# Kernel optimization log

Hardware: AMD Instinct MI355X
Metric: run time of the kernel (lower is better)

The kernel has to match this reference:

```python
import jax, jax.numpy as jnp
import numpy as np

B, T = 256, 512
D_L, D_T, D_W, D_S = 64, 32, 32, 32
XPRIME, HIDDEN = 256, 512


def setup_inputs() -> dict:
    key = jax.random.key(0)
    ks = jax.random.split(key, 11)
    s = 0.05
    return {
        "x_l_seq": jax.random.normal(ks[0], (B, T, D_L), jnp.float32),
        "x_t_seq": jax.random.normal(ks[1], (B, T, D_T), jnp.float32),
        "x_w_seq": jax.random.normal(ks[2], (B, T, D_W), jnp.float32),
        "x_s_seq": jax.random.normal(ks[3], (B, T, D_S), jnp.float32),
        "W_ih": jax.random.normal(ks[4], (3 * HIDDEN, XPRIME), jnp.float32) * s,
        "W_hh": jax.random.normal(ks[5], (3 * HIDDEN, HIDDEN), jnp.float32) * s,
        "b_ih": jax.random.normal(ks[6], (3 * HIDDEN,), jnp.float32) * s,
        "b_hh": jax.random.normal(ks[7], (3 * HIDDEN,), jnp.float32) * s,
        "Wt_h": jax.random.normal(ks[8], (XPRIME, HIDDEN), jnp.float32) * s,
        "Wt_x": jax.random.normal(ks[9], (XPRIME, D_L + D_T + D_W + D_S), jnp.float32) * s,
        "bt": jax.random.normal(ks[10], (XPRIME,), jnp.float32) * s,
    }


def reference(x_l_seq, x_t_seq, x_w_seq, x_s_seq, W_ih, W_hh, b_ih, b_hh, Wt_h, Wt_x, bt):
    # concat the four feature streams once: [B, T, D_tot]
    x_cat = jnp.concatenate([x_l_seq, x_t_seq, x_w_seq, x_s_seq], axis=-1)
    H = W_hh.shape[1]
    Bb = x_cat.shape[0]

    def step(h, x_t):  # h: [B,H], x_t: [B,D_tot]
        # transform_block: per-step meta transform fused with recurrence
        x_prime = jnp.tanh(h @ Wt_h.T + x_t @ Wt_x.T + bt)  # [B, XPRIME]
        # torch nn.GRU cell (gate order r, z, n)
        gx = x_prime @ W_ih.T + b_ih  # [B, 3H]
        gh = h @ W_hh.T + b_hh        # [B, 3H]
        xr, xz, xn = gx[:, :H], gx[:, H:2 * H], gx[:, 2 * H:]
        hr, hz, hn = gh[:, :H], gh[:, H:2 * H], gh[:, 2 * H:]
        r = jax.nn.sigmoid(xr + hr)
        z = jax.nn.sigmoid(xz + hz)
        n = jnp.tanh(xn + r * hn)
        h_new = (1.0 - z) * n + z * h
        return h_new, None

    h0 = jnp.zeros((Bb, H), x_cat.dtype)
    hT, _ = jax.lax.scan(step, h0, jnp.swapaxes(x_cat, 0, 1))  # scan over T
    return hT[None, :, :]  # [num_layers=1, B, H]
```

## Files before the change

### kernel.cpp

```cpp
#include <hip/hip_runtime.h>
#include <math.h>

typedef __attribute__((ext_vector_type(8))) short short8;
typedef __attribute__((ext_vector_type(4))) float floatx4;
typedef __attribute__((ext_vector_type(4))) unsigned uintx4;

#define NB 256
#define NH 512
#define NXP 256
#define NT 512
#define GHP 100

#define MFMA __builtin_amdgcn_mfma_f32_16x16x32_bf16

__device__ __forceinline__ unsigned short f2bf(float f) {
    union { float f; unsigned u; } x; x.f = f;
    unsigned r = x.u + 0x7FFFu + ((x.u >> 16) & 1u);
    return (unsigned short)(r >> 16);
}
__device__ __forceinline__ float sigmoidf_(float x) { return 1.0f / (1.0f + __expf(-x)); }

__device__ __forceinline__ short8 cvt8(float4 u, float4 v) {
    short8 r;
    r[0] = (short)f2bf(u.x); r[1] = (short)f2bf(u.y);
    r[2] = (short)f2bf(u.z); r[3] = (short)f2bf(u.w);
    r[4] = (short)f2bf(v.x); r[5] = (short)f2bf(v.y);
    r[6] = (short)f2bf(v.z); r[7] = (short)f2bf(v.w);
    return r;
}

__device__ __forceinline__ void ldg4_c(const void* p0, const void* p1,
                                       const void* p2, const void* p3,
                                       uintx4& r0, uintx4& r1, uintx4& r2, uintx4& r3) {
    asm volatile(
        "global_load_dwordx4 %0, %4, off sc0 sc1\n\t"
        "global_load_dwordx4 %1, %5, off sc0 sc1\n\t"
        "global_load_dwordx4 %2, %6, off sc0 sc1\n\t"
        "global_load_dwordx4 %3, %7, off sc0 sc1\n\t"
        "s_waitcnt vmcnt(0)"
        : "=&v"(r0), "=&v"(r1), "=&v"(r2), "=&v"(r3)
        : "v"(p0), "v"(p1), "v"(p2), "v"(p3) : "memory");
}
__device__ __forceinline__ void ldg2_c(const void* p0, const void* p1,
                                       uintx4& r0, uintx4& r1) {
    asm volatile(
        "global_load_dwordx4 %0, %2, off sc0 sc1\n\t"
        "global_load_dwordx4 %1, %3, off sc0 sc1\n\t"
        "s_waitcnt vmcnt(0)"
        : "=&v"(r0), "=&v"(r1) : "v"(p0), "v"(p1) : "memory");
}
__device__ __forceinline__ void st16_c(void* p, unsigned v) {
    asm volatile("global_store_short %0, %1, off sc0 sc1" :: "v"(p), "v"(v) : "memory");
}
__device__ __forceinline__ void st32_c(void* p, unsigned v) {
    asm volatile("global_store_dword %0, %1, off sc0 sc1" :: "v"(p), "v"(v) : "memory");
}
__device__ __forceinline__ void vm_drain() {
    asm volatile("s_waitcnt vmcnt(0)" ::: "memory");
}

__device__ __forceinline__ void flag_set(int* f, int v) {
    __hip_atomic_store(f, v, __ATOMIC_RELAXED, __HIP_MEMORY_SCOPE_AGENT);
}
__device__ __forceinline__ void poll16(const int* f, int target, int lane) {
    const int* fp = f + (lane & 15) * 16;
    for (;;) {
        int v = __hip_atomic_load(fp, __ATOMIC_RELAXED, __HIP_MEMORY_SCOPE_AGENT);
        if (__ballot(v < target) == 0ull) break;
        __builtin_amdgcn_s_sleep(1);
    }
}

__global__ void k_cvt(const float* __restrict__ src, unsigned short* __restrict__ dst, int n) {
    int i = blockIdx.x * blockDim.x + threadIdx.x;
    int stride = gridDim.x * blockDim.x;
    for (; i < n; i += stride) dst[i] = f2bf(src[i]);
}

struct KParams {
    const float *xl, *xt, *xw, *xs;
    const float *bih, *bhh, *bt;
    const unsigned short *Wihb, *Whhb, *Wthb, *Wtxb;
    unsigned short *hb0, *hb1, *xpb;
    float *out;
    int *flags;
};

__global__ __launch_bounds__(256, 1)
void k_persist(KParams P)
{
    const int tid   = threadIdx.x;
    const int w     = tid >> 6;
    const int lane  = tid & 63;
    const int lr    = lane & 15;
    const int lkrow = lane >> 4;
    const int lk    = lkrow * 8;
    const int bid   = blockIdx.x;
    const int grp   = bid >> 4;
    const int jc    = bid & 15;
    const int m0    = grp * 16;
    const int j0    = jc * 32;
    const int n0    = jc * 16;

    int* gfl = P.flags + grp * 512;
    int* hfl = gfl;
    int* xfl = gfl + 256;

    __shared__ unsigned short sh_h[16 * 512];
    __shared__ unsigned short sh_xp[16 * 256];
    __shared__ float sh_gh[16 * GHP];
    __shared__ float sh_gx[2][16 * GHP];
    __shared__ float sh_hf[16 * 32];
    __shared__ float sh_b[6][32];
    __shared__ float sh_bt[16];

    if (tid < 32) {
        sh_b[0][tid] = P.bih[j0 + tid];
        sh_b[1][tid] = P.bih[512 + j0 + tid];
        sh_b[2][tid] = P.bih[1024 + j0 + tid];
        sh_b[3][tid] = P.bhh[j0 + tid];
        sh_b[4][tid] = P.bhh[512 + j0 + tid];
        sh_b[5][tid] = P.bhh[1024 + j0 + tid];
    }
    if (tid < 16) sh_bt[tid] = P.bt[n0 + tid];
    sh_hf[tid] = 0.f; sh_hf[tid + 256] = 0.f;

    short8 bWih[3][4];
    short8 bWhh[2][16];
    #pragma unroll
    for (int i = 0; i < 3; ++i) {
        const int u = w * 3 + i, tile = u >> 1, kh = u & 1;
        const int g = tile >> 1, sub = tile & 1;
        const unsigned short* bp =
            P.Wihb + (size_t)(g * 512 + j0 + sub * 16 + lr) * NXP + kh * 128 + lk;
        #pragma unroll
        for (int kb = 0; kb < 4; ++kb) bWih[i][kb] = *(const short8*)(bp + kb * 32);
    }
    if (w < 3) {
        #pragma unroll
        for (int sub = 0; sub < 2; ++sub) {
            const unsigned short* bp =
                P.Whhb + (size_t)(w * 512 + j0 + sub * 16 + lr) * NH + lk;
            #pragma unroll
            for (int kb = 0; kb < 16; ++kb) bWhh[sub][kb] = *(const short8*)(bp + kb * 32);
        }
    } else {
        const unsigned short* bp = P.Wthb + (size_t)(n0 + lr) * NH + lk;
        #pragma unroll
        for (int kb = 0; kb < 16; ++kb) bWhh[0][kb] = *(const short8*)(bp + kb * 32);
        const unsigned short* bx = P.Wtxb + (size_t)(n0 + lr) * 160 + lk;
        #pragma unroll
        for (int c = 0; c < 5; ++c) bWhh[1][c] = *(const short8*)(bx + c * 32);
    }
    __syncthreads();

    for (int t = 0; t < NT; ++t) {
        const unsigned short* hsrc = (t & 1) ? P.hb1 : P.hb0;
        unsigned short*       hdst = (t & 1) ? P.hb0 : P.hb1;

        float4 xq[5][2];
        if (w == 3) {
            const size_t r = (size_t)(m0 + lr);
            #pragma unroll
            for (int c = 0; c < 5; ++c) {
                const float* pa = (c < 2) ? P.xl + (r * NT + t) * 64 + c * 32 + lk
                                : (c == 2)? P.xt + (r * NT + t) * 32 + lk
                                : (c == 3)? P.xw + (r * NT + t) * 32 + lk
                                          : P.xs + (r * NT + t) * 32 + lk;
                xq[c][0] = *(const float4*)pa;
                xq[c][1] = *(const float4*)(pa + 4);
            }
        }

        poll16(hfl, t, lane);
        {
            const int row = tid >> 4, c = (tid & 15) * 32;
            const unsigned short* gp = hsrc + (size_t)(m0 + row) * NH + c;
            uintx4 r0, r1, r2, r3;
            ldg4_c(gp, gp + 8, gp + 16, gp + 24, r0, r1, r2, r3);
            const int sw = (row & 7) * 8;
            *(uintx4*)&sh_h[row * 512 + ((c +  0) ^ sw)] = r0;
            *(uintx4*)&sh_h[row * 512 + ((c +  8) ^ sw)] = r1;
            *(uintx4*)&sh_h[row * 512 + ((c + 16) ^ sw)] = r2;
            *(uintx4*)&sh_h[row * 512 + ((c + 24) ^ sw)] = r3;
        }
        __syncthreads();

        if (w < 3) {
            floatx4 a0 = (floatx4){0.f,0.f,0.f,0.f};
            floatx4 a1 = (floatx4){0.f,0.f,0.f,0.f};
            const int sw = (lr & 7) * 8;
            #pragma unroll
            for (int kb = 0; kb < 16; ++kb) {
                short8 a = *(const short8*)&sh_h[lr * 512 + ((kb * 32 + lk) ^ sw)];
                a0 = MFMA(a, bWhh[0][kb], a0, 0, 0, 0);
                a1 = MFMA(a, bWhh[1][kb], a1, 0, 0, 0);
            }
            #pragma unroll
            for (int rg = 0; rg < 4; ++rg) {
                const int row = lkrow * 4 + rg;
                sh_gh[row * GHP + w * 32 + lr]      = a0[rg];
                sh_gh[row * GHP + w * 32 + 16 + lr] = a1[rg];
            }
        } else {
            floatx4 acc = (floatx4){0.f,0.f,0.f,0.f};
            const int sw = (lr & 7) * 8;
            #pragma unroll
            for (int kb = 0; kb < 16; ++kb) {
                short8 a = *(const short8*)&sh_h[lr * 512 + ((kb * 32 + lk) ^ sw)];
                acc = MFMA(a, bWhh[0][kb], acc, 0, 0, 0);
            }
            #pragma unroll
            for (int c = 0; c < 5; ++c) {
                short8 a = cvt8(xq[c][0], xq[c][1]);
                acc = MFMA(a, bWhh[1][c], acc, 0, 0, 0);
            }
            #pragma unroll
            for (int rg = 0; rg < 4; ++rg) {
                const int row = lkrow * 4 + rg;
                unsigned short v = f2bf(tanhf(acc[rg] + sh_bt[lr]));
                st16_c(P.xpb + (size_t)(m0 + row) * NXP + n0 + lr, (unsigned)v);
            }
            vm_drain();
            if (lane == 0) flag_set(xfl + jc * 16, t + 1);
        }

        poll16(xfl, t + 1, lane);
        {
            const int row = tid >> 4, c = (tid & 15) * 16;
            const unsigned short* gp = P.xpb + (size_t)(m0 + row) * NXP + c;
            uintx4 r0, r1;
            ldg2_c(gp, gp + 8, r0, r1);
            const int sw = (row & 7) * 8;
            *(uintx4*)&sh_xp[row * 256 + ((c + 0) ^ sw)] = r0;
            *(uintx4*)&sh_xp[row * 256 + ((c + 8) ^ sw)] = r1;
        }
        __syncthreads();

        #pragma unroll
        for (int i = 0; i < 3; ++i) {
            const int u = w * 3 + i, tile = u >> 1, kh = u & 1;
            const int g = tile >> 1, sub = tile & 1;
            floatx4 acc = (floatx4){0.f,0.f,0.f,0.f};
            const int sw = (lr & 7) * 8;
            #pragma unroll
            for (int kb = 0; kb < 4; ++kb) {
                short8 a = *(const short8*)&sh_xp[lr * 256 + ((kh * 128 + kb * 32 + lk) ^ sw)];
                acc = MFMA(a, bWih[i][kb], acc, 0, 0, 0);
            }
            #pragma unroll
            for (int rg = 0; rg < 4; ++rg) {
                const int row = lkrow * 4 + rg;
                sh_gx[kh][row * GHP + g * 32 + sub * 16 + lr] = acc[rg];
            }
        }
        __syncthreads();

        {
            const int row = tid >> 4, jj = (tid & 15) * 2;
            float hn[2];
            #pragma unroll
            for (int jo = 0; jo < 2; ++jo) {
                const int j = jj + jo;
                float gxr = sh_gx[0][row * GHP + j]      + sh_gx[1][row * GHP + j];
                float gxz = sh_gx[0][row * GHP + 32 + j] + sh_gx[1][row * GHP + 32 + j];
                float gxn = sh_gx[0][row * GHP + 64 + j] + sh_gx[1][row * GHP + 64 + j];
                float ghr = sh_gh[row * GHP + j];
                float ghz = sh_gh[row * GHP + 32 + j];
                float ghn = sh_gh[row * GHP + 64 + j];
                float rg_ = sigmoidf_(gxr + ghr + sh_b[0][j] + sh_b[3][j]);
                float zg  = sigmoidf_(gxz + ghz + sh_b[1][j] + sh_b[4][j]);
                float ng  = tanhf(gxn + sh_b[2][j] + rg_ * (ghn + sh_b[5][j]));
                float hold = sh_hf[row * 32 + j];
                hn[jo] = (1.f - zg) * ng + zg * hold;
                sh_hf[row * 32 + j] = hn[jo];
            }
            unsigned d = (unsigned)f2bf(hn[0]) | ((unsigned)f2bf(hn[1]) << 16);
            st32_c(hdst + (size_t)(m0 + row) * NH + j0 + jj, d);
            if (t == NT - 1) {
                float2 o; o.x = hn[0]; o.y = hn[1];
                *(float2*)&P.out[(size_t)(m0 + row) * NH + j0 + jj] = o;
            }
            vm_drain();
        }
        __syncthreads();
        if (tid == 0) flag_set(hfl + jc * 16, t + 1);
    }
}

extern "C" void kernel_launch(void* const* d_in, const int* in_sizes, int n_in,
                              void* d_out, int out_size, void* d_ws, size_t ws_size,
                              hipStream_t stream)
{
    (void)in_sizes; (void)n_in; (void)out_size;
    const float* xl  = (const float*)d_in[0];
    const float* xt_ = (const float*)d_in[1];
    const float* xw  = (const float*)d_in[2];
    const float* xs  = (const float*)d_in[3];
    const float* Wih = (const float*)d_in[4];
    const float* Whh = (const float*)d_in[5];
    const float* bih = (const float*)d_in[6];
    const float* bhh = (const float*)d_in[7];
    const float* Wth = (const float*)d_in[8];
    const float* Wtx = (const float*)d_in[9];
    const float* bt  = (const float*)d_in[10];

    char* p = (char*)d_ws;
    int* flags = (int*)p;                       p += 32768;
    unsigned short* hb0 = (unsigned short*)p;   p += (size_t)NB * NH * 2;
    unsigned short* hb1 = (unsigned short*)p;   p += (size_t)NB * NH * 2;
    unsigned short* xpb = (unsigned short*)p;   p += (size_t)NB * NXP * 2;
    unsigned short* Wihb = (unsigned short*)p;  p += (size_t)1536 * 256 * 2;
    unsigned short* Whhb = (unsigned short*)p;  p += (size_t)1536 * 512 * 2;
    unsigned short* Wthb = (unsigned short*)p;  p += (size_t)256 * 512 * 2;
    unsigned short* Wtxb = (unsigned short*)p;  p += (size_t)256 * 160 * 2;
    if ((size_t)(p - (char*)d_ws) > ws_size) return;

    k_cvt<<<256, 256, 0, stream>>>(Wih, Wihb, 1536 * 256);
    k_cvt<<<256, 256, 0, stream>>>(Whh, Whhb, 1536 * 512);
    k_cvt<<<64, 256, 0, stream>>>(Wth, Wthb, 256 * 512);
    k_cvt<<<32, 256, 0, stream>>>(Wtx, Wtxb, 256 * 160);
    hipMemsetAsync(flags, 0, 32768, stream);
    hipMemsetAsync(hb0, 0, (size_t)NB * NH * 2, stream);

    KParams P;
    P.xl = xl; P.xt = xt_; P.xw = xw; P.xs = xs;
    P.bih = bih; P.bhh = bhh; P.bt = bt;
    P.Wihb = Wihb; P.Whhb = Whhb; P.Wthb = Wthb; P.Wtxb = Wtxb;
    P.hb0 = hb0; P.hb1 = hb1; P.xpb = xpb;
    P.out = (float*)d_out; P.flags = flags;

    void* args[] = { &P };
    if (hipLaunchCooperativeKernel((const void*)k_persist, dim3(256), dim3(256),
                                   args, 0, stream) != hipSuccess) {
        k_persist<<<256, 256, 0, stream>>>(P);
    }
}
```

Measured before the change: 3.244 ms.

## Use 128 blocks of 512 threads, each covering 64 hidden columns

Halves the grid to 128 persistent blocks with 8 waves each, so every block handles 64 hidden columns and 32 x-prime columns instead of 32 and 16. Flag polling now runs in a single wave followed by a block barrier, and each wave publishes its own h flag instead of one flag per block after a final barrier. The goal is fewer cross-block dependencies and flags per step, with each block sharing the staged h rows over more work. The cost is half as many CUs in use, more register pressure at launch_bounds(512,2), and extra __syncthreads per step.

```diff
diff --git a/kernel.cpp b/kernel.cpp
--- a/kernel.cpp
+++ b/kernel.cpp
@@ -9,7 +9,7 @@
 #define NH 512
 #define NXP 256
 #define NT 512
-#define GHP 100
+#define GH2 200
 
 #define MFMA __builtin_amdgcn_mfma_f32_16x16x32_bf16
 
@@ -29,18 +29,6 @@
     return r;
 }
 
-__device__ __forceinline__ void ldg4_c(const void* p0, const void* p1,
-                                       const void* p2, const void* p3,
-                                       uintx4& r0, uintx4& r1, uintx4& r2, uintx4& r3) {
-    asm volatile(
-        "global_load_dwordx4 %0, %4, off sc0 sc1\n\t"
-        "global_load_dwordx4 %1, %5, off sc0 sc1\n\t"
-        "global_load_dwordx4 %2, %6, off sc0 sc1\n\t"
-        "global_load_dwordx4 %3, %7, off sc0 sc1\n\t"
-        "s_waitcnt vmcnt(0)"
-        : "=&v"(r0), "=&v"(r1), "=&v"(r2), "=&v"(r3)
-        : "v"(p0), "v"(p1), "v"(p2), "v"(p3) : "memory");
-}
 __device__ __forceinline__ void ldg2_c(const void* p0, const void* p1,
                                        uintx4& r0, uintx4& r1) {
     asm volatile(
@@ -49,6 +37,12 @@
         "s_waitcnt vmcnt(0)"
         : "=&v"(r0), "=&v"(r1) : "v"(p0), "v"(p1) : "memory");
 }
+__device__ __forceinline__ void ldg1_c(const void* p0, uintx4& r0) {
+    asm volatile(
+        "global_load_dwordx4 %0, %1, off sc0 sc1\n\t"
+        "s_waitcnt vmcnt(0)"
+        : "=&v"(r0) : "v"(p0) : "memory");
+}
 __device__ __forceinline__ void st16_c(void* p, unsigned v) {
     asm volatile("global_store_short %0, %1, off sc0 sc1" :: "v"(p), "v"(v) : "memory");
 }
@@ -61,6 +55,14 @@
 
 __device__ __forceinline__ void flag_set(int* f, int v) {
     __hip_atomic_store(f, v, __ATOMIC_RELAXED, __HIP_MEMORY_SCOPE_AGENT);
+}
+__device__ __forceinline__ void poll64(const int* f, int target, int lane) {
+    const int* fp = f + lane * 16;
+    for (;;) {
+        int v = __hip_atomic_load(fp, __ATOMIC_RELAXED, __HIP_MEMORY_SCOPE_AGENT);
+        if (__ballot(v < target) == 0ull) break;
+        __builtin_amdgcn_s_sleep(1);
+    }
 }
 __device__ __forceinline__ void poll16(const int* f, int target, int lane) {
     const int* fp = f + (lane & 15) * 16;
@@ -86,7 +88,7 @@
     int *flags;
 };
 
-__global__ __launch_bounds__(256, 1)
+__global__ __launch_bounds__(512, 2)
 void k_persist(KParams P)
 {
     const int tid   = threadIdx.x;
@@ -96,25 +98,25 @@
     const int lkrow = lane >> 4;
     const int lk    = lkrow * 8;
     const int bid   = blockIdx.x;
-    const int grp   = bid >> 4;
-    const int jc    = bid & 15;
+    const int grp   = bid >> 3;
+    const int jc    = bid & 7;
     const int m0    = grp * 16;
-    const int j0    = jc * 32;
-    const int n0    = jc * 16;
-
-    int* gfl = P.flags + grp * 512;
+    const int j0    = jc * 64;
+    const int n0    = jc * 32;
+
+    int* gfl = P.flags + grp * 2048;
     int* hfl = gfl;
-    int* xfl = gfl + 256;
+    int* xfl = gfl + 1024;
 
     __shared__ unsigned short sh_h[16 * 512];
     __shared__ unsigned short sh_xp[16 * 256];
-    __shared__ float sh_gh[16 * GHP];
-    __shared__ float sh_gx[2][16 * GHP];
-    __shared__ float sh_hf[16 * 32];
-    __shared__ float sh_b[6][32];
-    __shared__ float sh_bt[16];
-
-    if (tid < 32) {
+    __shared__ float sh_gh[16 * GH2];
+    __shared__ float sh_gx[2][16 * GH2];
+    __shared__ float sh_hf[16 * 64];
+    __shared__ float sh_b[6][64];
+    __shared__ float sh_bt[32];
+
+    if (tid < 64) {
         sh_b[0][tid] = P.bih[j0 + tid];
         sh_b[1][tid] = P.bih[512 + j0 + tid];
         sh_b[2][tid] = P.bih[1024 + j0 + tid];
@@ -122,35 +124,37 @@
         sh_b[4][tid] = P.bhh[512 + j0 + tid];
         sh_b[5][tid] = P.bhh[1024 + j0 + tid];
     }
-    if (tid < 16) sh_bt[tid] = P.bt[n0 + tid];
-    sh_hf[tid] = 0.f; sh_hf[tid + 256] = 0.f;
+    if (tid < 32) sh_bt[tid] = P.bt[n0 + tid];
+    sh_hf[tid] = 0.f; sh_hf[tid + 512] = 0.f;
 
     short8 bWih[3][4];
-    short8 bWhh[2][16];
+    short8 bW[2][16];
     #pragma unroll
     for (int i = 0; i < 3; ++i) {
         const int u = w * 3 + i, tile = u >> 1, kh = u & 1;
-        const int g = tile >> 1, sub = tile & 1;
+        const int g = tile >> 2, sub = tile & 3;
         const unsigned short* bp =
             P.Wihb + (size_t)(g * 512 + j0 + sub * 16 + lr) * NXP + kh * 128 + lk;
         #pragma unroll
         for (int kb = 0; kb < 4; ++kb) bWih[i][kb] = *(const short8*)(bp + kb * 32);
     }
-    if (w < 3) {
+    if (w < 6) {
+        const int g = w >> 1, cp = w & 1;
         #pragma unroll
         for (int sub = 0; sub < 2; ++sub) {
             const unsigned short* bp =
-                P.Whhb + (size_t)(w * 512 + j0 + sub * 16 + lr) * NH + lk;
-            #pragma unroll
-            for (int kb = 0; kb < 16; ++kb) bWhh[sub][kb] = *(const short8*)(bp + kb * 32);
+                P.Whhb + (size_t)(g * 512 + j0 + cp * 32 + sub * 16 + lr) * NH + lk;
+            #pragma unroll
+            for (int kb = 0; kb < 16; ++kb) bW[sub][kb] = *(const short8*)(bp + kb * 32);
         }
     } else {
-        const unsigned short* bp = P.Wthb + (size_t)(n0 + lr) * NH + lk;
-        #pragma unroll
-        for (int kb = 0; kb < 16; ++kb) bWhh[0][kb] = *(const short8*)(bp + kb * 32);
-        const unsigned short* bx = P.Wtxb + (size_t)(n0 + lr) * 160 + lk;
-        #pragma unroll
-        for (int c = 0; c < 5; ++c) bWhh[1][c] = *(const short8*)(bx + c * 32);
+        const int n = n0 + (w - 6) * 16;
+        const unsigned short* bp = P.Wthb + (size_t)(n + lr) * NH + lk;
+        #pragma unroll
+        for (int kb = 0; kb < 16; ++kb) bW[0][kb] = *(const short8*)(bp + kb * 32);
+        const unsigned short* bx = P.Wtxb + (size_t)(n + lr) * 160 + lk;
+        #pragma unroll
+        for (int c = 0; c < 5; ++c) bW[1][c] = *(const short8*)(bx + c * 32);
     }
     __syncthreads();
 
@@ -159,7 +163,7 @@
         unsigned short*       hdst = (t & 1) ? P.hb0 : P.hb1;
 
         float4 xq[5][2];
-        if (w == 3) {
+        if (w >= 6) {
             const size_t r = (size_t)(m0 + lr);
             #pragma unroll
             for (int c = 0; c < 5; ++c) {
@@ -172,35 +176,35 @@
             }
         }
 
-        poll16(hfl, t, lane);
+        if (w == 0) poll64(hfl, t, lane);
+        __syncthreads();
         {
-            const int row = tid >> 4, c = (tid & 15) * 32;
+            const int row = tid >> 5, c = (tid & 31) * 16;
             const unsigned short* gp = hsrc + (size_t)(m0 + row) * NH + c;
-            uintx4 r0, r1, r2, r3;
-            ldg4_c(gp, gp + 8, gp + 16, gp + 24, r0, r1, r2, r3);
+            uintx4 r0, r1;
+            ldg2_c(gp, gp + 8, r0, r1);
             const int sw = (row & 7) * 8;
-            *(uintx4*)&sh_h[row * 512 + ((c +  0) ^ sw)] = r0;
-            *(uintx4*)&sh_h[row * 512 + ((c +  8) ^ sw)] = r1;
-            *(uintx4*)&sh_h[row * 512 + ((c + 16) ^ sw)] = r2;
-            *(uintx4*)&sh_h[row * 512 + ((c + 24) ^ sw)] = r3;
-        }
-        __syncthreads();
-
-        if (w < 3) {
+            *(uintx4*)&sh_h[row * 512 + ((c + 0) ^ sw)] = r0;
+            *(uintx4*)&sh_h[row * 512 + ((c + 8) ^ sw)] = r1;
+        }
+        __syncthreads();
+
+        if (w < 6) {
+            const int g = w >> 1, cp = w & 1;
             floatx4 a0 = (floatx4){0.f,0.f,0.f,0.f};
             floatx4 a1 = (floatx4){0.f,0.f,0.f,0.f};
             const int sw = (lr & 7) * 8;
             #pragma unroll
             for (int kb = 0; kb < 16; ++kb) {
                 short8 a = *(const short8*)&sh_h[lr * 512 + ((kb * 32 + lk) ^ sw)];
-                a0 = MFMA(a, bWhh[0][kb], a0, 0, 0, 0);
-                a1 = MFMA(a, bWhh[1][kb], a1, 0, 0, 0);
+                a0 = MFMA(a, bW[0][kb], a0, 0, 0, 0);
+                a1 = MFMA(a, bW[1][kb], a1, 0, 0, 0);
             }
             #pragma unroll
             for (int rg = 0; rg < 4; ++rg) {
                 const int row = lkrow * 4 + rg;
-                sh_gh[row * GHP + w * 32 + lr]      = a0[rg];
-                sh_gh[row * GHP + w * 32 + 16 + lr] = a1[rg];
+                sh_gh[row * GH2 + g * 64 + cp * 32 + lr]      = a0[rg];
+                sh_gh[row * GH2 + g * 64 + cp * 32 + 16 + lr] = a1[rg];
             }
         } else {
             floatx4 acc = (floatx4){0.f,0.f,0.f,0.f};
@@ -208,39 +212,40 @@
             #pragma unroll
             for (int kb = 0; kb < 16; ++kb) {
                 short8 a = *(const short8*)&sh_h[lr * 512 + ((kb * 32 + lk) ^ sw)];
-                acc = MFMA(a, bWhh[0][kb], acc, 0, 0, 0);
+                acc = MFMA(a, bW[0][kb], acc, 0, 0, 0);
             }
             #pragma unroll
             for (int c = 0; c < 5; ++c) {
                 short8 a = cvt8(xq[c][0], xq[c][1]);
-                acc = MFMA(a, bWhh[1][c], acc, 0, 0, 0);
-            }
+                acc = MFMA(a, bW[1][c], acc, 0, 0, 0);
+            }
+            const int xcol = n0 + (w - 6) * 16 + lr;
             #pragma unroll
             for (int rg = 0; rg < 4; ++rg) {
                 const int row = lkrow * 4 + rg;
-                unsigned short v = f2bf(tanhf(acc[rg] + sh_bt[lr]));
-                st16_c(P.xpb + (size_t)(m0 + row) * NXP + n0 + lr, (unsigned)v);
+                unsigned short v = f2bf(tanhf(acc[rg] + sh_bt[(w - 6) * 16 + lr]));
+                st16_c(P.xpb + (size_t)(m0 + row) * NXP + xcol, (unsigned)v);
             }
             vm_drain();
-            if (lane == 0) flag_set(xfl + jc * 16, t + 1);
-        }
-
-        poll16(xfl, t + 1, lane);
+            if (lane == 0) flag_set(xfl + (jc * 2 + (w - 6)) * 16, t + 1);
+        }
+
+        if (w == 0) poll16(xfl, t + 1, lane);
+        __syncthreads();
         {
-            const int row = tid >> 4, c = (tid & 15) * 16;
+            const int row = tid >> 5, c = (tid & 31) * 8;
             const unsigned short* gp = P.xpb + (size_t)(m0 + row) * NXP + c;
-            uintx4 r0, r1;
-            ldg2_c(gp, gp + 8, r0, r1);
+            uintx4 r0;
+            ldg1_c(gp, r0);
             const int sw = (row & 7) * 8;
-            *(uintx4*)&sh_xp[row * 256 + ((c + 0) ^ sw)] = r0;
-            *(uintx4*)&sh_xp[row * 256 + ((c + 8) ^ sw)] = r1;
+            *(uintx4*)&sh_xp[row * 256 + (c ^ sw)] = r0;
         }
         __syncthreads();
 
         #pragma unroll
         for (int i = 0; i < 3; ++i) {
             const int u = w * 3 + i, tile = u >> 1, kh = u & 1;
-            const int g = tile >> 1, sub = tile & 1;
+            const int g = tile >> 2, sub = tile & 3;
             floatx4 acc = (floatx4){0.f,0.f,0.f,0.f};
             const int sw = (lr & 7) * 8;
             #pragma unroll
@@ -251,40 +256,39 @@
             #pragma unroll
             for (int rg = 0; rg < 4; ++rg) {
                 const int row = lkrow * 4 + rg;
-                sh_gx[kh][row * GHP + g * 32 + sub * 16 + lr] = acc[rg];
+                sh_gx[kh][row * GH2 + g * 64 + sub * 16 + lr] = acc[rg];
             }
         }
         __syncthreads();
 
         {
-            const int row = tid >> 4, jj = (tid & 15) * 2;
+            const int row = tid >> 5, jl = (tid & 31) * 2;
             float hn[2];
             #pragma unroll
             for (int jo = 0; jo < 2; ++jo) {
-                const int j = jj + jo;
-                float gxr = sh_gx[0][row * GHP + j]      + sh_gx[1][row * GHP + j];
-                float gxz = sh_gx[0][row * GHP + 32 + j] + sh_gx[1][row * GHP + 32 + j];
-                float gxn = sh_gx[0][row * GHP + 64 + j] + sh_gx[1][row * GHP + 64 + j];
-                float ghr = sh_gh[row * GHP + j];
-                float ghz = sh_gh[row * GHP + 32 + j];
-                float ghn = sh_gh[row * GHP + 64 + j];
+                const int j = jl + jo;
+                float gxr = sh_gx[0][row * GH2 + j]       + sh_gx[1][row * GH2 + j];
+                float gxz = sh_gx[0][row * GH2 + 64 + j]  + sh_gx[1][row * GH2 + 64 + j];
+                float gxn = sh_gx[0][row * GH2 + 128 + j] + sh_gx[1][row * GH2 + 128 + j];
+                float ghr = sh_gh[row * GH2 + j];
+                float ghz = sh_gh[row * GH2 + 64 + j];
+                float ghn = sh_gh[row * GH2 + 128 + j];
                 float rg_ = sigmoidf_(gxr + ghr + sh_b[0][j] + sh_b[3][j]);
                 float zg  = sigmoidf_(gxz + ghz + sh_b[1][j] + sh_b[4][j]);
                 float ng  = tanhf(gxn + sh_b[2][j] + rg_ * (ghn + sh_b[5][j]));
-                float hold = sh_hf[row * 32 + j];
+                float hold = sh_hf[row * 64 + j];
                 hn[jo] = (1.f - zg) * ng + zg * hold;
-                sh_hf[row * 32 + j] = hn[jo];
+                sh_hf[row * 64 + j] = hn[jo];
             }
             unsigned d = (unsigned)f2bf(hn[0]) | ((unsigned)f2bf(hn[1]) << 16);
-            st32_c(hdst + (size_t)(m0 + row) * NH + j0 + jj, d);
+            st32_c(hdst + (size_t)(m0 + row) * NH + j0 + jl, d);
             if (t == NT - 1) {
                 float2 o; o.x = hn[0]; o.y = hn[1];
-                *(float2*)&P.out[(size_t)(m0 + row) * NH + j0 + jj] = o;
+                *(float2*)&P.out[(size_t)(m0 + row) * NH + j0 + jl] = o;
             }
             vm_drain();
-        }
-        __syncthreads();
-        if (tid == 0) flag_set(hfl + jc * 16, t + 1);
+            if (lane == 0) flag_set(hfl + (jc * 8 + w) * 16, t + 1);
+        }
     }
 }
 
@@ -306,7 +310,7 @@
     const float* bt  = (const float*)d_in[10];
 
     char* p = (char*)d_ws;
-    int* flags = (int*)p;                       p += 32768;
+    int* flags = (int*)p;                       p += 16 * 2048 * 4;
     unsigned short* hb0 = (unsigned short*)p;   p += (size_t)NB * NH * 2;
     unsigned short* hb1 = (unsigned short*)p;   p += (size_t)NB * NH * 2;
     unsigned short* xpb = (unsigned short*)p;   p += (size_t)NB * NXP * 2;
@@ -320,7 +324,7 @@
     k_cvt<<<256, 256, 0, stream>>>(Whh, Whhb, 1536 * 512);
     k_cvt<<<64, 256, 0, stream>>>(Wth, Wthb, 256 * 512);
     k_cvt<<<32, 256, 0, stream>>>(Wtx, Wtxb, 256 * 160);
-    hipMemsetAsync(flags, 0, 32768, stream);
+    hipMemsetAsync(flags, 0, 16 * 2048 * 4, stream);
     hipMemsetAsync(hb0, 0, (size_t)NB * NH * 2, stream);
 
     KParams P;
@@ -331,8 +335,8 @@
     P.out = (float*)d_out; P.flags = flags;
 
     void* args[] = { &P };
-    if (hipLaunchCooperativeKernel((const void*)k_persist, dim3(256), dim3(256),
+    if (hipLaunchCooperativeKernel((const void*)k_persist, dim3(128), dim3(512),
                                    args, 0, stream) != hipSuccess) {
-        k_persist<<<256, 256, 0, stream>>>(P);
-    }
-}
+        k_persist<<<128, 512, 0, stream>>>(P);
+    }
+}
```

After: 3.794 ms. 17.0% more time.

## Replace flag-based inter-block sync with tag-embedded data polling

Applied to the files above, without the earlier changes.

Removes the separate flag arrays and the store-drain-flag handshake between blocks. Each bf16 value of h and x_prime is now stored in a 32-bit word whose upper 16 bits carry the step tag, and consumers poll the data itself until every word carries the expected tag, then repack to bf16 in shared memory. This cuts a round trip (drain, flag write, flag poll, then data load) from the critical path of every step, and also drops the trailing __syncthreads. In exchange it doubles the size of the exchanged buffers and adds repeated polling loads. Correctness rests on the tag staying unique across the double buffer; the 16-bit tag only ever reaches 512, so that holds here.

```diff
diff --git a/kernel.cpp b/kernel.cpp
--- a/kernel.cpp
+++ b/kernel.cpp
@@ -29,46 +29,15 @@
     return r;
 }
 
-__device__ __forceinline__ void ldg4_c(const void* p0, const void* p1,
-                                       const void* p2, const void* p3,
-                                       uintx4& r0, uintx4& r1, uintx4& r2, uintx4& r3) {
-    asm volatile(
-        "global_load_dwordx4 %0, %4, off sc0 sc1\n\t"
-        "global_load_dwordx4 %1, %5, off sc0 sc1\n\t"
-        "global_load_dwordx4 %2, %6, off sc0 sc1\n\t"
-        "global_load_dwordx4 %3, %7, off sc0 sc1\n\t"
-        "s_waitcnt vmcnt(0)"
-        : "=&v"(r0), "=&v"(r1), "=&v"(r2), "=&v"(r3)
-        : "v"(p0), "v"(p1), "v"(p2), "v"(p3) : "memory");
-}
-__device__ __forceinline__ void ldg2_c(const void* p0, const void* p1,
-                                       uintx4& r0, uintx4& r1) {
-    asm volatile(
-        "global_load_dwordx4 %0, %2, off sc0 sc1\n\t"
-        "global_load_dwordx4 %1, %3, off sc0 sc1\n\t"
-        "s_waitcnt vmcnt(0)"
-        : "=&v"(r0), "=&v"(r1) : "v"(p0), "v"(p1) : "memory");
-}
-__device__ __forceinline__ void st16_c(void* p, unsigned v) {
-    asm volatile("global_store_short %0, %1, off sc0 sc1" :: "v"(p), "v"(v) : "memory");
+__device__ __forceinline__ void ldg4_nw(const void* p, uintx4& r) {
+    asm volatile("global_load_dwordx4 %0, %1, off sc0 sc1"
+                 : "=&v"(r) : "v"(p) : "memory");
 }
 __device__ __forceinline__ void st32_c(void* p, unsigned v) {
     asm volatile("global_store_dword %0, %1, off sc0 sc1" :: "v"(p), "v"(v) : "memory");
 }
 __device__ __forceinline__ void vm_drain() {
     asm volatile("s_waitcnt vmcnt(0)" ::: "memory");
-}
-
-__device__ __forceinline__ void flag_set(int* f, int v) {
-    __hip_atomic_store(f, v, __ATOMIC_RELAXED, __HIP_MEMORY_SCOPE_AGENT);
-}
-__device__ __forceinline__ void poll16(const int* f, int target, int lane) {
-    const int* fp = f + (lane & 15) * 16;
-    for (;;) {
-        int v = __hip_atomic_load(fp, __ATOMIC_RELAXED, __HIP_MEMORY_SCOPE_AGENT);
-        if (__ballot(v < target) == 0ull) break;
-        __builtin_amdgcn_s_sleep(1);
-    }
 }
 
 __global__ void k_cvt(const float* __restrict__ src, unsigned short* __restrict__ dst, int n) {
@@ -81,9 +50,8 @@
     const float *xl, *xt, *xw, *xs;
     const float *bih, *bhh, *bt;
     const unsigned short *Wihb, *Whhb, *Wthb, *Wtxb;
-    unsigned short *hb0, *hb1, *xpb;
+    unsigned *hT0, *hT1, *xT;
     float *out;
-    int *flags;
 };
 
 __global__ __launch_bounds__(256, 1)
@@ -102,10 +70,6 @@
     const int j0    = jc * 32;
     const int n0    = jc * 16;
 
-    int* gfl = P.flags + grp * 512;
-    int* hfl = gfl;
-    int* xfl = gfl + 256;
-
     __shared__ unsigned short sh_h[16 * 512];
     __shared__ unsigned short sh_xp[16 * 256];
     __shared__ float sh_gh[16 * GHP];
@@ -155,8 +119,8 @@
     __syncthreads();
 
     for (int t = 0; t < NT; ++t) {
-        const unsigned short* hsrc = (t & 1) ? P.hb1 : P.hb0;
-        unsigned short*       hdst = (t & 1) ? P.hb0 : P.hb1;
+        const unsigned* hTs = (t & 1) ? P.hT1 : P.hT0;
+        unsigned*       hTd = (t & 1) ? P.hT0 : P.hT1;
 
         float4 xq[5][2];
         if (w == 3) {
@@ -172,17 +136,38 @@
             }
         }
 
-        poll16(hfl, t, lane);
         {
             const int row = tid >> 4, c = (tid & 15) * 32;
-            const unsigned short* gp = hsrc + (size_t)(m0 + row) * NH + c;
-            uintx4 r0, r1, r2, r3;
-            ldg4_c(gp, gp + 8, gp + 16, gp + 24, r0, r1, r2, r3);
+            const unsigned* bp = hTs + (size_t)(m0 + row) * NH + c;
+            uintx4 B[8];
+            unsigned pend = 0xFFu;
+            const unsigned tg = (unsigned)t;
+            for (;;) {
+                #pragma unroll
+                for (int b = 0; b < 8; ++b)
+                    if (pend & (1u << b)) ldg4_nw(bp + b * 4, B[b]);
+                vm_drain();
+                __builtin_amdgcn_sched_barrier(0);
+                #pragma unroll
+                for (int b = 0; b < 8; ++b)
+                    if (pend & (1u << b)) {
+                        if ((B[b][0] >> 16) == tg && (B[b][1] >> 16) == tg &&
+                            (B[b][2] >> 16) == tg && (B[b][3] >> 16) == tg)
+                            pend &= ~(1u << b);
+                    }
+                if (__ballot(pend != 0u) == 0ull) break;
+                __builtin_amdgcn_s_sleep(1);
+            }
             const int sw = (row & 7) * 8;
-            *(uintx4*)&sh_h[row * 512 + ((c +  0) ^ sw)] = r0;
-            *(uintx4*)&sh_h[row * 512 + ((c +  8) ^ sw)] = r1;
-            *(uintx4*)&sh_h[row * 512 + ((c + 16) ^ sw)] = r2;
-            *(uintx4*)&sh_h[row * 512 + ((c + 24) ^ sw)] = r3;
+            #pragma unroll
+            for (int q = 0; q < 4; ++q) {
+                uintx4 pk;
+                pk[0] = (B[2*q][0]   & 0xffffu) | (B[2*q][1]   << 16);
+                pk[1] = (B[2*q][2]   & 0xffffu) | (B[2*q][3]   << 16);
+                pk[2] = (B[2*q+1][0] & 0xffffu) | (B[2*q+1][1] << 16);
+                pk[3] = (B[2*q+1][2] & 0xffffu) | (B[2*q+1][3] << 16);
+                *(uintx4*)&sh_h[row * 512 + ((c + 8 * q) ^ sw)] = pk;
+            }
         }
         __syncthreads();
 
@@ -215,25 +200,47 @@
                 short8 a = cvt8(xq[c][0], xq[c][1]);
                 acc = MFMA(a, bWhh[1][c], acc, 0, 0, 0);
             }
+            const unsigned xtag = ((unsigned)(t + 1)) << 16;
             #pragma unroll
             for (int rg = 0; rg < 4; ++rg) {
                 const int row = lkrow * 4 + rg;
                 unsigned short v = f2bf(tanhf(acc[rg] + sh_bt[lr]));
-                st16_c(P.xpb + (size_t)(m0 + row) * NXP + n0 + lr, (unsigned)v);
-            }
-            vm_drain();
-            if (lane == 0) flag_set(xfl + jc * 16, t + 1);
-        }
-
-        poll16(xfl, t + 1, lane);
+                st32_c(P.xT + (size_t)(m0 + row) * NXP + n0 + lr, xtag | (unsigned)v);
+            }
+        }
+
         {
             const int row = tid >> 4, c = (tid & 15) * 16;
-            const unsigned short* gp = P.xpb + (size_t)(m0 + row) * NXP + c;
-            uintx4 r0, r1;
-            ldg2_c(gp, gp + 8, r0, r1);
+            const unsigned* bp = P.xT + (size_t)(m0 + row) * NXP + c;
+            uintx4 B[4];
+            unsigned pend = 0xFu;
+            const unsigned tg = (unsigned)(t + 1);
+            for (;;) {
+                #pragma unroll
+                for (int b = 0; b < 4; ++b)
+                    if (pend & (1u << b)) ldg4_nw(bp + b * 4, B[b]);
+                vm_drain();
+                __builtin_amdgcn_sched_barrier(0);
+                #pragma unroll
+                for (int b = 0; b < 4; ++b)
+                    if (pend & (1u << b)) {
+                        if ((B[b][0] >> 16) == tg && (B[b][1] >> 16) == tg &&
+                            (B[b][2] >> 16) == tg && (B[b][3] >> 16) == tg)
+                            pend &= ~(1u << b);
+                    }
+                if (__ballot(pend != 0u) == 0ull) break;
+                __builtin_amdgcn_s_sleep(1);
+            }
             const int sw = (row & 7) * 8;
-            *(uintx4*)&sh_xp[row * 256 + ((c + 0) ^ sw)] = r0;
-            *(uintx4*)&sh_xp[row * 256 + ((c + 8) ^ sw)] = r1;
+            #pragma unroll
+            for (int q = 0; q < 2; ++q) {
+                uintx4 pk;
+                pk[0] = (B[2*q][0]   & 0xffffu) | (B[2*q][1]   << 16);
+                pk[1] = (B[2*q][2]   & 0xffffu) | (B[2*q][3]   << 16);
+                pk[2] = (B[2*q+1][0] & 0xffffu) | (B[2*q+1][1] << 16);
+                pk[3] = (B[2*q+1][2] & 0xffffu) | (B[2*q+1][3] << 16);
+                *(uintx4*)&sh_xp[row * 256 + ((c + 8 * q) ^ sw)] = pk;
+            }
         }
         __syncthreads();
 
@@ -275,16 +282,15 @@
                 hn[jo] = (1.f - zg) * ng + zg * hold;
                 sh_hf[row * 32 + j] = hn[jo];
             }
-            unsigned d = (unsigned)f2bf(hn[0]) | ((unsigned)f2bf(hn[1]) << 16);
-            st32_c(hdst + (size_t)(m0 + row) * NH + j0 + jj, d);
+            const unsigned htag = ((unsigned)(t + 1)) << 16;
+            unsigned* hp = hTd + (size_t)(m0 + row) * NH + j0 + jj;
+            st32_c(hp,     htag | (unsigned)f2bf(hn[0]));
+            st32_c(hp + 1, htag | (unsigned)f2bf(hn[1]));
             if (t == NT - 1) {
                 float2 o; o.x = hn[0]; o.y = hn[1];
                 *(float2*)&P.out[(size_t)(m0 + row) * NH + j0 + jj] = o;
             }
-            vm_drain();
-        }
-        __syncthreads();
-        if (tid == 0) flag_set(hfl + jc * 16, t + 1);
+        }
     }
 }
 
@@ -306,10 +312,9 @@
     const float* bt  = (const float*)d_in[10];
 
     char* p = (char*)d_ws;
-    int* flags = (int*)p;                       p += 32768;
-    unsigned short* hb0 = (unsigned short*)p;   p += (size_t)NB * NH * 2;
-    unsigned short* hb1 = (unsigned short*)p;   p += (size_t)NB * NH * 2;
-    unsigned short* xpb = (unsigned short*)p;   p += (size_t)NB * NXP * 2;
+    unsigned* hT0 = (unsigned*)p;               p += (size_t)NB * NH * 4;
+    unsigned* hT1 = (unsigned*)p;               p += (size_t)NB * NH * 4;
+    unsigned* xT  = (unsigned*)p;               p += (size_t)NB * NXP * 4;
     unsigned short* Wihb = (unsigned short*)p;  p += (size_t)1536 * 256 * 2;
     unsigned short* Whhb = (unsigned short*)p;  p += (size_t)1536 * 512 * 2;
     unsigned short* Wthb = (unsigned short*)p;  p += (size_t)256 * 512 * 2;
@@ -320,15 +325,16 @@
     k_cvt<<<256, 256, 0, stream>>>(Whh, Whhb, 1536 * 512);
     k_cvt<<<64, 256, 0, stream>>>(Wth, Wthb, 256 * 512);
     k_cvt<<<32, 256, 0, stream>>>(Wtx, Wtxb, 256 * 160);
-    hipMemsetAsync(flags, 0, 32768, stream);
-    hipMemsetAsync(hb0, 0, (size_t)NB * NH * 2, stream);
+    hipMemsetAsync(hT0, 0, (size_t)NB * NH * 4, stream);
+    hipMemsetAsync(hT1, 0, (size_t)NB * NH * 4, stream);
+    hipMemsetAsync(xT,  0, (size_t)NB * NXP * 4, stream);
 
     KParams P;
     P.xl = xl; P.xt = xt_; P.xw = xw; P.xs = xs;
     P.bih = bih; P.bhh = bhh; P.bt = bt;
     P.Wihb = Wihb; P.Whhb = Whhb; P.Wthb = Wthb; P.Wtxb = Wtxb;
-    P.hb0 = hb0; P.hb1 = hb1; P.xpb = xpb;
-    P.out = (float*)d_out; P.flags = flags;
+    P.hT0 = hT0; P.hT1 = hT1; P.xT = xT;
+    P.out = (float*)d_out;
 
     void* args[] = { &P };
     if (hipLaunchCooperativeKernel((const void*)k_persist, dim3(256), dim3(256),
```

After: 4.612 ms. 1.42x slower.

## Concentrate x_prime production in four blocks per group, poll four flags

Applied to the files above, without the earlier changes.

Previously each of the 16 blocks in a row group had its fourth wave compute 16 columns of x_prime and set its own flag, so consumers polled 16 flags. Now only the first 4 blocks per group compute x_prime, with all four waves each producing 16 columns (64 per block), and consumers poll just 4 flags. The aim is to shorten the cross-block dependency chain and polling cost on the critical path of the recurrence. In exchange, the producer blocks take on extra work and an added block barrier before the W_hh matmul, which can make them stragglers, and each thread holds 21 more register vectors.

```diff
diff --git a/kernel.cpp b/kernel.cpp
--- a/kernel.cpp
+++ b/kernel.cpp
@@ -64,6 +64,14 @@
 }
 __device__ __forceinline__ void poll16(const int* f, int target, int lane) {
     const int* fp = f + (lane & 15) * 16;
+    for (;;) {
+        int v = __hip_atomic_load(fp, __ATOMIC_RELAXED, __HIP_MEMORY_SCOPE_AGENT);
+        if (__ballot(v < target) == 0ull) break;
+        __builtin_amdgcn_s_sleep(1);
+    }
+}
+__device__ __forceinline__ void poll4(const int* f, int target, int lane) {
+    const int* fp = f + (lane & 3) * 16;
     for (;;) {
         int v = __hip_atomic_load(fp, __ATOMIC_RELAXED, __HIP_MEMORY_SCOPE_AGENT);
         if (__ballot(v < target) == 0ull) break;
@@ -100,7 +108,8 @@
     const int jc    = bid & 15;
     const int m0    = grp * 16;
     const int j0    = jc * 32;
-    const int n0    = jc * 16;
+    const bool xprod = (jc < 4);
+    const int xn    = jc * 64 + w * 16;
 
     int* gfl = P.flags + grp * 512;
     int* hfl = gfl;
@@ -112,7 +121,7 @@
     __shared__ float sh_gx[2][16 * GHP];
     __shared__ float sh_hf[16 * 32];
     __shared__ float sh_b[6][32];
-    __shared__ float sh_bt[16];
+    __shared__ float sh_bt[64];
 
     if (tid < 32) {
         sh_b[0][tid] = P.bih[j0 + tid];
@@ -122,11 +131,12 @@
         sh_b[4][tid] = P.bhh[512 + j0 + tid];
         sh_b[5][tid] = P.bhh[1024 + j0 + tid];
     }
-    if (tid < 16) sh_bt[tid] = P.bt[n0 + tid];
+    if (xprod && tid < 64) sh_bt[tid] = P.bt[jc * 64 + tid];
     sh_hf[tid] = 0.f; sh_hf[tid + 256] = 0.f;
 
     short8 bWih[3][4];
     short8 bWhh[2][16];
+    short8 bWt[21];
     #pragma unroll
     for (int i = 0; i < 3; ++i) {
         const int u = w * 3 + i, tile = u >> 1, kh = u & 1;
@@ -144,13 +154,14 @@
             #pragma unroll
             for (int kb = 0; kb < 16; ++kb) bWhh[sub][kb] = *(const short8*)(bp + kb * 32);
         }
-    } else {
-        const unsigned short* bp = P.Wthb + (size_t)(n0 + lr) * NH + lk;
-        #pragma unroll
-        for (int kb = 0; kb < 16; ++kb) bWhh[0][kb] = *(const short8*)(bp + kb * 32);
-        const unsigned short* bx = P.Wtxb + (size_t)(n0 + lr) * 160 + lk;
-        #pragma unroll
-        for (int c = 0; c < 5; ++c) bWhh[1][c] = *(const short8*)(bx + c * 32);
+    }
+    if (xprod) {
+        const unsigned short* bp = P.Wthb + (size_t)(xn + lr) * NH + lk;
+        #pragma unroll
+        for (int kb = 0; kb < 16; ++kb) bWt[kb] = *(const short8*)(bp + kb * 32);
+        const unsigned short* bx = P.Wtxb + (size_t)(xn + lr) * 160 + lk;
+        #pragma unroll
+        for (int c = 0; c < 5; ++c) bWt[16 + c] = *(const short8*)(bx + c * 32);
     }
     __syncthreads();
 
@@ -159,7 +170,7 @@
         unsigned short*       hdst = (t & 1) ? P.hb0 : P.hb1;
 
         float4 xq[5][2];
-        if (w == 3) {
+        if (xprod) {
             const size_t r = (size_t)(m0 + lr);
             #pragma unroll
             for (int c = 0; c < 5; ++c) {
@@ -186,6 +197,30 @@
         }
         __syncthreads();
 
+        if (xprod) {
+            floatx4 acc = (floatx4){0.f,0.f,0.f,0.f};
+            const int sw = (lr & 7) * 8;
+            #pragma unroll
+            for (int kb = 0; kb < 16; ++kb) {
+                short8 a = *(const short8*)&sh_h[lr * 512 + ((kb * 32 + lk) ^ sw)];
+                acc = MFMA(a, bWt[kb], acc, 0, 0, 0);
+            }
+            #pragma unroll
+            for (int c = 0; c < 5; ++c) {
+                short8 a = cvt8(xq[c][0], xq[c][1]);
+                acc = MFMA(a, bWt[16 + c], acc, 0, 0, 0);
+            }
+            #pragma unroll
+            for (int rg = 0; rg < 4; ++rg) {
+                const int row = lkrow * 4 + rg;
+                unsigned short v = f2bf(tanhf(acc[rg] + sh_bt[w * 16 + lr]));
+                st16_c(P.xpb + (size_t)(m0 + row) * NXP + xn + lr, (unsigned)v);
+            }
+            vm_drain();
+        }
+        __syncthreads();
+        if (xprod && tid == 0) flag_set(xfl + jc * 16, t + 1);
+
         if (w < 3) {
             floatx4 a0 = (floatx4){0.f,0.f,0.f,0.f};
             floatx4 a1 = (floatx4){0.f,0.f,0.f,0.f};
@@ -202,30 +237,9 @@
                 sh_gh[row * GHP + w * 32 + lr]      = a0[rg];
                 sh_gh[row * GHP + w * 32 + 16 + lr] = a1[rg];
             }
-        } else {
-            floatx4 acc = (floatx4){0.f,0.f,0.f,0.f};
-            const int sw = (lr & 7) * 8;
-            #pragma unroll
-            for (int kb = 0; kb < 16; ++kb) {
-                short8 a = *(const short8*)&sh_h[lr * 512 + ((kb * 32 + lk) ^ sw)];
-                acc = MFMA(a, bWhh[0][kb], acc, 0, 0, 0);
-            }
-            #pragma unroll
-            for (int c = 0; c < 5; ++c) {
-                short8 a = cvt8(xq[c][0], xq[c][1]);
-                acc = MFMA(a, bWhh[1][c], acc, 0, 0, 0);
-            }
-            #pragma unroll
-            for (int rg = 0; rg < 4; ++rg) {
-                const int row = lkrow * 4 + rg;
-                unsigned short v = f2bf(tanhf(acc[rg] + sh_bt[lr]));
-                st16_c(P.xpb + (size_t)(m0 + row) * NXP + n0 + lr, (unsigned)v);
-            }
-            vm_drain();
-            if (lane == 0) flag_set(xfl + jc * 16, t + 1);
-        }
-
-        poll16(xfl, t + 1, lane);
+        }
+
+        poll4(xfl, t + 1, lane);
         {
             const int row = tid >> 4, c = (tid & 15) * 16;
             const unsigned short* gp = P.xpb + (size_t)(m0 + row) * NXP + c;
```

After: 3.545 ms. +9.3%, slower.
